# Performance work log

Hardware: AMD Instinct MI355X
Metric: run time of the kernel (lower is better)

## Reference

```python
import jax, jax.numpy as jnp
import numpy as np

D = 256      # word_embd_size
V = 32000    # vocab_size_w
B, T, J = 32, 512, 128


def _gru_dir(x, wih, whh, bih, bhh):
    # x: (B, T, D); torch GRU cell convention
    def step(h, xt):
        gi = xt @ wih.T + bih            # (B, 3D)
        gh = h @ whh.T + bhh
        i_r, i_z, i_n = jnp.split(gi, 3, axis=-1)
        h_r, h_z, h_n = jnp.split(gh, 3, axis=-1)
        r = jax.nn.sigmoid(i_r + h_r)
        z = jax.nn.sigmoid(i_z + h_z)
        n = jnp.tanh(i_n + r * h_n)
        h_new = (1.0 - z) * n + z * h
        return h_new, h_new
    h0 = jnp.zeros((x.shape[0], D), dtype=x.dtype)
    _, ys = jax.lax.scan(step, h0, jnp.swapaxes(x, 0, 1))
    return jnp.swapaxes(ys, 0, 1)         # (B, T, D)


def _bigru(x, wih_f, whh_f, bih_f, bhh_f, wih_b, whh_b, bih_b, bhh_b):
    fwd = _gru_dir(x, wih_f, whh_f, bih_f, bhh_f)
    bwd = jnp.flip(_gru_dir(jnp.flip(x, 1), wih_b, whh_b, bih_b, bhh_b), 1)
    return jnp.concatenate([fwd, bwd], axis=-1)   # (B, T, 2D)


def _cmnt_sim(ctx, cmnt_e, action, w2):
    # Fused form of: S = W2_ha(cat(ctx_ex * cmnt_ex, action_ex)) over (B,T,J,2D+1)
    # S[b,t,j] = sum_d ctx[b,t,d]*cmnt[b,j,d]*w2[d] + action[b,t]*w2[2D]
    S = jnp.einsum('btd,bjd->btj', ctx * w2[:2 * D], cmnt_e)
    S = S + action.astype(ctx.dtype)[:, :, None] * w2[2 * D]
    b = jax.nn.softmax(jnp.max(S, axis=2), axis=-1)   # (B, T)
    return jnp.einsum('bt,btj->bj', b, S)             # (B, J)


def setup_inputs() -> dict:
    key = jax.random.key(0)
    ks = jax.random.split(key, 20)
    s = 1.0 / np.sqrt(D)
    u = lambda k, shape: jax.random.uniform(k, shape, minval=-s, maxval=s, dtype=jnp.float32)
    return {
        'cmnt': jax.random.randint(ks[0], (B, J), 0, V),
        'src_token': jax.random.randint(ks[1], (B, T), 0, V),
        'tgt_token': jax.random.randint(ks[2], (B, T), 0, V),
        'src_action': jax.random.randint(ks[3], (B, T), 0, 2),
        'tgt_action': jax.random.randint(ks[4], (B, T), 0, 2),
        'emb': jax.random.normal(ks[5], (V, D), dtype=jnp.float32) * 0.02,
        'wih_f': u(ks[6], (3 * D, D)), 'whh_f': u(ks[7], (3 * D, D)),
        'bih_f': u(ks[8], (3 * D,)),  'bhh_f': u(ks[9], (3 * D,)),
        'wih_b': u(ks[10], (3 * D, D)), 'whh_b': u(ks[11], (3 * D, D)),
        'bih_b': u(ks[12], (3 * D,)),  'bhh_b': u(ks[13], (3 * D,)),
        'w2': u(ks[14], (2 * D + 1,)),
        'rank_w': u(ks[15], (2 * J, 1)),
        'rank_b': u(ks[16], (1,)),
    }


def reference(cmnt, src_token, tgt_token, src_action, tgt_action, emb,
              wih_f, whh_f, bih_f, bhh_f, wih_b, whh_b, bih_b, bhh_b,
              w2, rank_w, rank_b):
    gru = lambda x: _bigru(x, wih_f, whh_f, bih_f, bhh_f, wih_b, whh_b, bih_b, bhh_b)
    e_src = gru(emb[src_token])    # (B, T, 2D)
    e_tgt = gru(emb[tgt_token])    # (B, T, 2D)
    e_cmnt = gru(emb[cmnt])        # (B, J, 2D)
    S_src = _cmnt_sim(e_src, e_cmnt, src_action, w2)
    S_tgt = _cmnt_sim(e_tgt, e_cmnt, tgt_action, w2)
    S_diff = jnp.concatenate([S_src, S_tgt], axis=1)   # (B, 2J)
    result = S_diff @ rank_w + rank_b                   # (B, 1)
    return result, S_diff
```

## Files before the change

kernel.cpp:

```cpp
#include <hip/hip_runtime.h>
#include <math.h>

#define DD   256
#define TTT  512
#define JJJ  128
#define BBB  32
#define NC   1536
#define ROWS_ALL 36864

typedef _Float16 v2h __attribute__((ext_vector_type(2)));
typedef _Float16 v4h __attribute__((ext_vector_type(4)));
typedef short short8 __attribute__((ext_vector_type(8)));
typedef float f32x4 __attribute__((ext_vector_type(4)));

#if __has_builtin(__builtin_amdgcn_fdot2)
#define FDOT2(a, b, c) __builtin_amdgcn_fdot2((a), (b), (c), false)
#else
#define FDOT2(a, b, c) ((float)(a)[0] * (float)(b)[0] + ((float)(a)[1] * (float)(b)[1] + (c)))
#endif

__device__ __forceinline__ short f2bf(float f) {
    unsigned u = __float_as_uint(f);
    unsigned r = (u + 0x7FFFu + ((u >> 16) & 1u)) >> 16;
    return (short)r;
}

__global__ __launch_bounds__(256) void prep_kernel(
    const int* __restrict__ cmnt, const int* __restrict__ src_tok, const int* __restrict__ tgt_tok,
    const float* __restrict__ wih_f, const float* __restrict__ wih_b,
    const float* __restrict__ whh_f, const float* __restrict__ whh_b,
    const float* __restrict__ bih_f, const float* __restrict__ bih_b,
    const float* __restrict__ bhh_f, const float* __restrict__ bhh_b,
    int* __restrict__ tok_all, float* __restrict__ whhT,
    float* __restrict__ bihc, float* __restrict__ bhhc, short* __restrict__ Bt)
{
    const int idx = blockIdx.x * blockDim.x + threadIdx.x;
    const int stride = gridDim.x * blockDim.x;
    for (int i = idx; i < ROWS_ALL; i += stride)
        tok_all[i] = (i < 16384) ? src_tok[i] : (i < 32768) ? tgt_tok[i - 16384] : cmnt[i - 32768];
    for (int i = idx; i < 256 * NC; i += stride) {
        const int k = i / NC, c = i % NC;
        whhT[i] = (c < 768) ? whh_f[(size_t)c * 256 + k] : whh_b[(size_t)(c - 768) * 256 + k];
    }
    for (int i = idx; i < 393216; i += stride)
        Bt[i] = f2bf(i < 196608 ? wih_f[i] : wih_b[i - 196608]);
    for (int i = idx; i < NC; i += stride) {
        bihc[i] = (i < 768) ? bih_f[i] : bih_b[i - 768];
        bhhc[i] = (i < 768) ? bhh_f[i] : bhh_b[i - 768];
    }
}

__global__ __launch_bounds__(256) void gatherA_kernel(
    const int* __restrict__ tok, int row_start, int nrows,
    const float* __restrict__ emb, short* __restrict__ A)
{
    const int idx = blockIdx.x * blockDim.x + threadIdx.x;
    const int stride = gridDim.x * blockDim.x;
    const int ngroups = nrows * 64;
    for (int g = idx; g < ngroups; g += stride) {
        const int i = g >> 6;
        const int kq = (g & 63) << 2;
        const float4 v = *(const float4*)(emb + (size_t)tok[row_start + i] * 256 + kq);
        short4 s;
        s.x = f2bf(v.x); s.y = f2bf(v.y); s.z = f2bf(v.z); s.w = f2bf(v.w);
        *(short4*)(A + (size_t)i * 256 + kq) = s;
    }
}

#define LP 40
__global__ __launch_bounds__(256) void gi_mfma(
    const short* __restrict__ A, const short* __restrict__ Bt,
    const float* __restrict__ bihc, _Float16* __restrict__ gi)
{
    __shared__ __align__(16) short As[128 * LP];
    __shared__ __align__(16) short Bs[128 * LP];
    const int tid = threadIdx.x;
    const int wave = tid >> 6, lane = tid & 63;
    const int quad = lane >> 4, l16 = lane & 15;
    const int m0 = blockIdx.x * 128, n0 = blockIdx.y * 128;
    const int wm = (wave & 1) * 64, wn = (wave >> 1) * 64;

    const int sr = tid >> 2;
    const int sk = (tid & 3) * 8;
    const short* ga0 = A  + (size_t)(m0 + sr) * 256 + sk;
    const short* ga1 = A  + (size_t)(m0 + sr + 64) * 256 + sk;
    const short* gb0 = Bt + (size_t)(n0 + sr) * 256 + sk;
    const short* gb1 = Bt + (size_t)(n0 + sr + 64) * 256 + sk;

    f32x4 acc[4][4];
    #pragma unroll
    for (int i = 0; i < 4; ++i)
        #pragma unroll
        for (int j = 0; j < 4; ++j) acc[i][j] = (f32x4){0.f, 0.f, 0.f, 0.f};

    for (int k0 = 0; k0 < 256; k0 += 32) {
        const short8 a0 = *(const short8*)(ga0 + k0);
        const short8 a1 = *(const short8*)(ga1 + k0);
        const short8 b0 = *(const short8*)(gb0 + k0);
        const short8 b1 = *(const short8*)(gb1 + k0);
        __syncthreads();
        *(short8*)&As[sr * LP + sk] = a0;
        *(short8*)&As[(sr + 64) * LP + sk] = a1;
        *(short8*)&Bs[sr * LP + sk] = b0;
        *(short8*)&Bs[(sr + 64) * LP + sk] = b1;
        __syncthreads();
        short8 af[4], bf[4];
        #pragma unroll
        for (int i = 0; i < 4; ++i)
            af[i] = *(const short8*)&As[(wm + i * 16 + l16) * LP + quad * 8];
        #pragma unroll
        for (int j = 0; j < 4; ++j)
            bf[j] = *(const short8*)&Bs[(wn + j * 16 + l16) * LP + quad * 8];
        #pragma unroll
        for (int i = 0; i < 4; ++i)
            #pragma unroll
            for (int j = 0; j < 4; ++j)
                acc[i][j] = __builtin_amdgcn_mfma_f32_16x16x32_bf16(af[i], bf[j], acc[i][j], 0, 0, 0);
    }

    #pragma unroll
    for (int j = 0; j < 4; ++j) {
        const int col = n0 + wn + j * 16 + l16;
        const float bias = bihc[col];
        #pragma unroll
        for (int i = 0; i < 4; ++i) {
            const int r0 = m0 + wm + i * 16 + quad * 4;
            #pragma unroll
            for (int reg = 0; reg < 4; ++reg)
                gi[(size_t)(r0 + reg) * NC + col] = (_Float16)(acc[i][j][reg] + bias);
        }
    }
}

__global__ __launch_bounds__(512, 2) void gru_kernel(
    const _Float16* __restrict__ gi0, const _Float16* __restrict__ gi1, const _Float16* __restrict__ gi2,
    const float* __restrict__ whhT, const float* __restrict__ bhhc,
    _Float16* __restrict__ e_src, _Float16* __restrict__ e_tgt, _Float16* __restrict__ e_cmnt,
    int chain_base)
{
    const int chain = chain_base + (int)(blockIdx.x >> 5);
    const int b = (int)(blockIdx.x & 31);
    const int seq = chain >> 1, dir = chain & 1;
    const int Tlen = (seq == 2) ? JJJ : TTT;
    const _Float16* gi = (seq == 0) ? gi0 : (seq == 1) ? gi1 : gi2;
    _Float16* e = (seq == 0) ? e_src : (seq == 1) ? e_tgt : e_cmnt;

    const int tid = threadIdx.x;
    const int j = tid & 255;
    const int q = tid >> 8;
    const int cb = dir * 768;

    __shared__ __align__(16) v2h h2s[128];
    __shared__ float parts[3][256];

    v2h wr2[64], wz2[64], wn2[64];
    {
        const float* wb = whhT + (size_t)(q * 128) * NC + cb + j;
        #pragma unroll
        for (int p = 0; p < 64; ++p) {
            v2h a, bzv, c;
            a[0]   = (_Float16)wb[0];        a[1]   = (_Float16)wb[NC];
            bzv[0] = (_Float16)wb[256];      bzv[1] = (_Float16)wb[NC + 256];
            c[0]   = (_Float16)wb[512];      c[1]   = (_Float16)wb[NC + 512];
            wr2[p] = a; wz2[p] = bzv; wn2[p] = c;
            wb += 2 * NC;
        }
    }
    const float br  = bhhc[cb + j];
    const float bzb = bhhc[cb + 256 + j];
    const float bnb = bhhc[cb + 512 + j];

    float hprev = 0.f;
    if (q == 0 && (j & 1) == 0) {
        v2h z0; z0[0] = (_Float16)0.f; z0[1] = (_Float16)0.f;
        h2s[j >> 1] = z0;
    }
    __syncthreads();

    const int t0i = dir ? (Tlen - 1) : 0;
    const long tstep = dir ? -1 : 1;
    const _Float16* girow = gi + (size_t)(b * Tlen + t0i) * NC + cb;
    _Float16* eptr = e + (size_t)(b * Tlen + t0i) * 512 + (dir << 8) + j;
    const long gstep = tstep * NC;
    const long estep = tstep * 512;

    for (int s = 0; s < Tlen; ++s) {
        float gr_ = 0.f, gz_ = 0.f, gn_ = 0.f;
        if (q == 0) {
            gr_ = (float)girow[j];
            gz_ = (float)girow[256 + j];
            gn_ = (float)girow[512 + j];
        }

        float ar = 0.f, az = 0.f, an = 0.f;
        const v2h* hbase = &h2s[q * 64];
        #pragma unroll
        for (int c = 0; c < 16; ++c) {
            union { float4 f; v2h h[4]; } U;
            U.f = *(const float4*)&hbase[c * 4];
            #pragma unroll
            for (int p = 0; p < 4; ++p) {
                ar = FDOT2(wr2[c * 4 + p], U.h[p], ar);
                az = FDOT2(wz2[c * 4 + p], U.h[p], az);
                an = FDOT2(wn2[c * 4 + p], U.h[p], an);
            }
        }
        if (q == 1) { parts[0][j] = ar; parts[1][j] = az; parts[2][j] = an; }
        __syncthreads();

        if (q == 0) {
            const float sr = ar + parts[0][j] + br;
            const float sz = az + parts[1][j] + bzb;
            const float sn = an + parts[2][j] + bnb;
            const float r = 1.f / (1.f + __expf(-(gr_ + sr)));
            const float z = 1.f / (1.f + __expf(-(gz_ + sz)));
            const float n = tanhf(gn_ + r * sn);
            const float hnew = (1.f - z) * n + z * hprev;
            hprev = hnew;
            *eptr = (_Float16)hnew;
            const float hnb = __shfl_xor(hnew, 1);
            if ((j & 1) == 0) {
                v2h hv; hv[0] = (_Float16)hnew; hv[1] = (_Float16)hnb;
                h2s[j >> 1] = hv;
            }
        }
        girow += gstep;
        eptr += estep;
        __syncthreads();
    }
}

__global__ __launch_bounds__(256) void sim_gemm(
    const _Float16* __restrict__ e_src, const _Float16* __restrict__ e_tgt,
    const _Float16* __restrict__ e_cmnt, const float* __restrict__ w2,
    const int* __restrict__ src_action, const int* __restrict__ tgt_action,
    float* __restrict__ S, float* __restrict__ rowmaxP)
{
    const int seq = (int)(blockIdx.z >> 5);
    const int b = (int)(blockIdx.z & 31);
    const int t0 = blockIdx.x * 64;
    const int j0 = blockIdx.y * 64;
    const _Float16* ctx = ((seq == 0) ? e_src : e_tgt) + (size_t)b * 512 * 512;
    const _Float16* ec = e_cmnt + (size_t)b * 128 * 512;
    const int* act = (seq == 0) ? src_action : tgt_action;

    __shared__ __align__(16) float As[16][68];
    __shared__ __align__(16) float Bs[16][68];
    const int tid = threadIdx.x;
    const int lr = tid >> 2;
    const int lk = (tid & 3) << 2;
    const int ty = tid >> 4, tx = tid & 15;
    float acc[4][4];
    #pragma unroll
    for (int i = 0; i < 4; ++i)
        #pragma unroll
        for (int q = 0; q < 4; ++q) acc[i][q] = 0.f;

    for (int k0 = 0; k0 < 512; k0 += 16) {
        const float4 w4 = *(const float4*)(w2 + k0 + lk);
        const v4h a4 = *(const v4h*)(ctx + (size_t)(t0 + lr) * 512 + k0 + lk);
        const v4h b4 = *(const v4h*)(ec + (size_t)(j0 + lr) * 512 + k0 + lk);
        __syncthreads();
        As[lk + 0][lr] = (float)a4[0] * w4.x; As[lk + 1][lr] = (float)a4[1] * w4.y;
        As[lk + 2][lr] = (float)a4[2] * w4.z; As[lk + 3][lr] = (float)a4[3] * w4.w;
        Bs[lk + 0][lr] = (float)b4[0]; Bs[lk + 1][lr] = (float)b4[1];
        Bs[lk + 2][lr] = (float)b4[2]; Bs[lk + 3][lr] = (float)b4[3];
        __syncthreads();
        #pragma unroll
        for (int kk = 0; kk < 16; ++kk) {
            const float4 av = *(const float4*)&As[kk][ty * 4];
            const float4 bv = *(const float4*)&Bs[kk][tx * 4];
            float a[4] = {av.x, av.y, av.z, av.w};
            float bb[4] = {bv.x, bv.y, bv.z, bv.w};
            #pragma unroll
            for (int i = 0; i < 4; ++i)
                #pragma unroll
                for (int q = 0; q < 4; ++q) acc[i][q] = fmaf(a[i], bb[q], acc[i][q]);
        }
    }
    const float w2a = w2[512];
    #pragma unroll
    for (int i = 0; i < 4; ++i) {
        const int t = t0 + ty * 4 + i;
        const float aterm = (float)act[b * 512 + t] * w2a;
        float4 o;
        o.x = acc[i][0] + aterm; o.y = acc[i][1] + aterm;
        o.z = acc[i][2] + aterm; o.w = acc[i][3] + aterm;
        *(float4*)(S + ((size_t)((seq * 32 + b) * 512 + t)) * 128 + j0 + tx * 4) = o;
        float m = fmaxf(fmaxf(o.x, o.y), fmaxf(o.z, o.w));
        m = fmaxf(m, __shfl_xor(m, 1));
        m = fmaxf(m, __shfl_xor(m, 2));
        m = fmaxf(m, __shfl_xor(m, 4));
        m = fmaxf(m, __shfl_xor(m, 8));
        if (tx == 0)
            rowmaxP[(size_t)blockIdx.y * 32768 + (seq * 32 + b) * 512 + t] = m;
    }
}

__global__ __launch_bounds__(256) void softmax_kernel(const float* __restrict__ rowmaxP, float* __restrict__ bw)
{
    const int base = blockIdx.x * 512;
    const int tid = threadIdx.x;
    __shared__ float red[256];
    const float v0 = fmaxf(rowmaxP[base + tid], rowmaxP[32768 + base + tid]);
    const float v1 = fmaxf(rowmaxP[base + 256 + tid], rowmaxP[32768 + base + 256 + tid]);
    red[tid] = fmaxf(v0, v1);
    __syncthreads();
    for (int off = 128; off > 0; off >>= 1) {
        if (tid < off) red[tid] = fmaxf(red[tid], red[tid + off]);
        __syncthreads();
    }
    const float M = red[0];
    __syncthreads();
    const float e0 = __expf(v0 - M), e1 = __expf(v1 - M);
    red[tid] = e0 + e1;
    __syncthreads();
    for (int off = 128; off > 0; off >>= 1) {
        if (tid < off) red[tid] += red[tid + off];
        __syncthreads();
    }
    const float inv = 1.f / red[0];
    bw[base + tid] = e0 * inv;
    bw[base + 256 + tid] = e1 * inv;
}

__global__ __launch_bounds__(256) void weighted_kernel(
    const float* __restrict__ S, const float* __restrict__ bw, float* __restrict__ outSP)
{
    const int sb = blockIdx.x;
    const int ch = blockIdx.y;
    const int tid = threadIdx.x;
    const int j = tid & 127, half = tid >> 7;
    const float* Sb = S + (size_t)sb * 512 * 128;
    const float* w = bw + sb * 512;
    const int tb = ch * 64 + half * 32;
    float acc = 0.f;
    for (int t = tb; t < tb + 32; ++t)
        acc = fmaf(w[t], Sb[(size_t)t * 128 + j], acc);
    __shared__ float red[256];
    red[tid] = acc;
    __syncthreads();
    if (half == 0) outSP[(size_t)ch * 8192 + sb * 128 + j] = red[j] + red[128 + j];
}

__global__ __launch_bounds__(256) void final_kernel(
    const float* __restrict__ outSP, const float* __restrict__ rank_w,
    const float* __restrict__ rank_b, float* __restrict__ out)
{
    __shared__ float sArr[8192];
    const int tid = threadIdx.x;
    for (int q = tid; q < 8192; q += 256) {
        float s = 0.f;
        #pragma unroll
        for (int c = 0; c < 8; ++c) s += outSP[(size_t)c * 8192 + q];
        sArr[q] = s;
    }
    __syncthreads();
    for (int q = tid; q < 8192; q += 256) {
        const int b = q >> 8, c = q & 255;
        out[32 + q] = (c < 128) ? sArr[b * 128 + c] : sArr[4096 + b * 128 + (c - 128)];
    }
    if (tid < 32) {
        float acc = rank_b[0];
        for (int c = 0; c < 128; ++c) acc = fmaf(sArr[tid * 128 + c], rank_w[c], acc);
        for (int c = 0; c < 128; ++c) acc = fmaf(sArr[4096 + tid * 128 + c], rank_w[128 + c], acc);
        out[tid] = acc;
    }
}

extern "C" void kernel_launch(void* const* d_in, const int* in_sizes, int n_in,
                              void* d_out, int out_size, void* d_ws, size_t ws_size,
                              hipStream_t stream)
{
    const int* cmnt       = (const int*)d_in[0];
    const int* src_token  = (const int*)d_in[1];
    const int* tgt_token  = (const int*)d_in[2];
    const int* src_action = (const int*)d_in[3];
    const int* tgt_action = (const int*)d_in[4];
    const float* emb    = (const float*)d_in[5];
    const float* wih_f  = (const float*)d_in[6];
    const float* whh_f  = (const float*)d_in[7];
    const float* bih_f  = (const float*)d_in[8];
    const float* bhh_f  = (const float*)d_in[9];
    const float* wih_b  = (const float*)d_in[10];
    const float* whh_b  = (const float*)d_in[11];
    const float* bih_b  = (const float*)d_in[12];
    const float* bhh_b  = (const float*)d_in[13];
    const float* w2     = (const float*)d_in[14];
    const float* rank_w = (const float*)d_in[15];
    const float* rank_b = (const float*)d_in[16];
    float* out = (float*)d_out;

    float* ws = (float*)d_ws;
    size_t off = 0;
    int*   tok_all = (int*)(ws + off); off += 36864;
    short* Bt_bf16 = (short*)(ws + off); off += 196608;
    float* whhT   = ws + off; off += 393216;
    float* bihc   = ws + off; off += 1536;
    float* bhhc   = ws + off; off += 1536;
    float* rowmaxP = ws + off; off += 65536;
    float* bw     = ws + off; off += 32768;
    float* outSP  = ws + off; off += 65536;
    _Float16* e_src  = (_Float16*)(ws + off); off += 4194304;
    _Float16* e_tgt  = (_Float16*)(ws + off); off += 4194304;
    _Float16* e_cmnt = (_Float16*)(ws + off); off += 1048576;
    float* S      = ws + off; off += 4194304;
    _Float16* gih = (_Float16*)(ws + off);
    const size_t avail = ws_size / 4 - off;
    const bool planP = avail >= 28311552ULL;

    hipLaunchKernelGGL(prep_kernel, dim3(512), dim3(256), 0, stream,
        cmnt, src_token, tgt_token, wih_f, wih_b, whh_f, whh_b,
        bih_f, bih_b, bhh_f, bhh_b, tok_all, whhT, bihc, bhhc, Bt_bf16);

    if (planP) {
        short* A = (short*)e_src;
        hipLaunchKernelGGL(gatherA_kernel, dim3(4096), dim3(256), 0, stream,
            tok_all, 0, 36864, emb, A);
        hipLaunchKernelGGL(gi_mfma, dim3(288, 12), dim3(256), 0, stream,
            A, Bt_bf16, bihc, gih);
        hipLaunchKernelGGL(gru_kernel, dim3(192), dim3(512), 0, stream,
            gih, gih + (size_t)16384 * NC, gih + (size_t)32768 * NC,
            whhT, bhhc, e_src, e_tgt, e_cmnt, 0);
    } else {
        short* A = (short*)S;
        const int starts[3] = {0, 16384, 32768};
        const int nrows[3]  = {16384, 16384, 4096};
        for (int sq = 0; sq < 3; ++sq) {
            hipLaunchKernelGGL(gatherA_kernel, dim3(4096), dim3(256), 0, stream,
                tok_all, starts[sq], nrows[sq], emb, A);
            hipLaunchKernelGGL(gi_mfma, dim3(nrows[sq] / 128, 12), dim3(256), 0, stream,
                A, Bt_bf16, bihc, gih);
            hipLaunchKernelGGL(gru_kernel, dim3(64), dim3(512), 0, stream,
                gih, gih, gih, whhT, bhhc, e_src, e_tgt, e_cmnt, 2 * sq);
        }
    }

    hipLaunchKernelGGL(sim_gemm, dim3(8, 2, 64), dim3(256), 0, stream,
        e_src, e_tgt, e_cmnt, w2, src_action, tgt_action, S, rowmaxP);
    hipLaunchKernelGGL(softmax_kernel, dim3(64), dim3(256), 0, stream, rowmaxP, bw);
    hipLaunchKernelGGL(weighted_kernel, dim3(64, 8), dim3(256), 0, stream, S, bw, outSP);
    hipLaunchKernelGGL(final_kernel, dim3(1), dim3(256), 0, stream, outSP, rank_w, rank_b, out);
}
```

Measured before the change: 895.8 us.

## Port similarity GEMM to fp16 MFMA, defer GRU stores, use expf tanh

Replaces the scalar-FMA similarity GEMM with a 128x128-tile MFMA kernel using fp16 operands, with w2 pre-converted to fp16 and multiplied into the context rows in half precision. In the GRU recurrence, each step's global store of h is deferred to the start of the next step so it overlaps the next gate loads. tanhf is replaced by an exp-based formula. These cut FMA throughput cost and per-step latency on the sequential GRU path, but the fp16 product of context and w2 and the fast tanh lower accuracy.

```diff
diff --git a/kernel.cpp b/kernel.cpp
--- a/kernel.cpp
+++ b/kernel.cpp
@@ -10,6 +10,7 @@
 
 typedef _Float16 v2h __attribute__((ext_vector_type(2)));
 typedef _Float16 v4h __attribute__((ext_vector_type(4)));
+typedef _Float16 v8h __attribute__((ext_vector_type(8)));
 typedef short short8 __attribute__((ext_vector_type(8)));
 typedef float f32x4 __attribute__((ext_vector_type(4)));
 
@@ -31,8 +32,10 @@
     const float* __restrict__ whh_f, const float* __restrict__ whh_b,
     const float* __restrict__ bih_f, const float* __restrict__ bih_b,
     const float* __restrict__ bhh_f, const float* __restrict__ bhh_b,
+    const float* __restrict__ w2,
     int* __restrict__ tok_all, float* __restrict__ whhT,
-    float* __restrict__ bihc, float* __restrict__ bhhc, short* __restrict__ Bt)
+    float* __restrict__ bihc, float* __restrict__ bhhc, short* __restrict__ Bt,
+    _Float16* __restrict__ w2h)
 {
     const int idx = blockIdx.x * blockDim.x + threadIdx.x;
     const int stride = gridDim.x * blockDim.x;
@@ -48,6 +51,8 @@
         bihc[i] = (i < 768) ? bih_f[i] : bih_b[i - 768];
         bhhc[i] = (i < 768) ? bhh_f[i] : bhh_b[i - 768];
     }
+    for (int i = idx; i < 512; i += stride)
+        w2h[i] = (_Float16)w2[i];
 }
 
 __global__ __launch_bounds__(256) void gatherA_kernel(
@@ -184,9 +189,13 @@
     const long gstep = tstep * NC;
     const long estep = tstep * 512;
 
+    _Float16* pptr = eptr;
+    float pval = 0.f;
+
     for (int s = 0; s < Tlen; ++s) {
         float gr_ = 0.f, gz_ = 0.f, gn_ = 0.f;
         if (q == 0) {
+            if (s > 0) *pptr = (_Float16)pval;
             gr_ = (float)girow[j];
             gz_ = (float)girow[256 + j];
             gn_ = (float)girow[512 + j];
@@ -214,10 +223,12 @@
             const float sn = an + parts[2][j] + bnb;
             const float r = 1.f / (1.f + __expf(-(gr_ + sr)));
             const float z = 1.f / (1.f + __expf(-(gz_ + sz)));
-            const float n = tanhf(gn_ + r * sn);
+            const float xa = gn_ + r * sn;
+            const float texp = __expf(2.f * xa);
+            const float n = 1.f - 2.f / (texp + 1.f);
             const float hnew = (1.f - z) * n + z * hprev;
             hprev = hnew;
-            *eptr = (_Float16)hnew;
+            pptr = eptr; pval = hnew;
             const float hnb = __shfl_xor(hnew, 1);
             if ((j & 1) == 0) {
                 v2h hv; hv[0] = (_Float16)hnew; hv[1] = (_Float16)hnb;
@@ -228,72 +239,92 @@
         eptr += estep;
         __syncthreads();
     }
-}
-
-__global__ __launch_bounds__(256) void sim_gemm(
+    if (q == 0) *pptr = (_Float16)pval;
+}
+
+__global__ __launch_bounds__(256) void sim_mfma(
     const _Float16* __restrict__ e_src, const _Float16* __restrict__ e_tgt,
-    const _Float16* __restrict__ e_cmnt, const float* __restrict__ w2,
+    const _Float16* __restrict__ e_cmnt, const _Float16* __restrict__ w2h,
+    const float* __restrict__ w2,
     const int* __restrict__ src_action, const int* __restrict__ tgt_action,
     float* __restrict__ S, float* __restrict__ rowmaxP)
 {
-    const int seq = (int)(blockIdx.z >> 5);
-    const int b = (int)(blockIdx.z & 31);
-    const int t0 = blockIdx.x * 64;
-    const int j0 = blockIdx.y * 64;
+    const int sb = (int)blockIdx.z;
+    const int seq = sb >> 5, b = sb & 31;
+    const int t0 = blockIdx.x * 128;
     const _Float16* ctx = ((seq == 0) ? e_src : e_tgt) + (size_t)b * 512 * 512;
     const _Float16* ec = e_cmnt + (size_t)b * 128 * 512;
     const int* act = (seq == 0) ? src_action : tgt_action;
 
-    __shared__ __align__(16) float As[16][68];
-    __shared__ __align__(16) float Bs[16][68];
-    const int tid = threadIdx.x;
-    const int lr = tid >> 2;
-    const int lk = (tid & 3) << 2;
-    const int ty = tid >> 4, tx = tid & 15;
-    float acc[4][4];
+    __shared__ __align__(16) _Float16 As[128 * LP];
+    __shared__ __align__(16) _Float16 Bs[128 * LP];
+    const int tid = threadIdx.x;
+    const int wave = tid >> 6, lane = tid & 63;
+    const int quad = lane >> 4, l16 = lane & 15;
+    const int wm = (wave & 1) * 64, wn = (wave >> 1) * 64;
+    const int sr = tid >> 2;
+    const int sk = (tid & 3) * 8;
+
+    const _Float16* ga0 = ctx + (size_t)(t0 + sr) * 512 + sk;
+    const _Float16* ga1 = ctx + (size_t)(t0 + sr + 64) * 512 + sk;
+    const _Float16* gb0 = ec + (size_t)sr * 512 + sk;
+    const _Float16* gb1 = ec + (size_t)(sr + 64) * 512 + sk;
+
+    f32x4 acc[4][4];
     #pragma unroll
     for (int i = 0; i < 4; ++i)
         #pragma unroll
-        for (int q = 0; q < 4; ++q) acc[i][q] = 0.f;
-
-    for (int k0 = 0; k0 < 512; k0 += 16) {
-        const float4 w4 = *(const float4*)(w2 + k0 + lk);
-        const v4h a4 = *(const v4h*)(ctx + (size_t)(t0 + lr) * 512 + k0 + lk);
-        const v4h b4 = *(const v4h*)(ec + (size_t)(j0 + lr) * 512 + k0 + lk);
-        __syncthreads();
-        As[lk + 0][lr] = (float)a4[0] * w4.x; As[lk + 1][lr] = (float)a4[1] * w4.y;
-        As[lk + 2][lr] = (float)a4[2] * w4.z; As[lk + 3][lr] = (float)a4[3] * w4.w;
-        Bs[lk + 0][lr] = (float)b4[0]; Bs[lk + 1][lr] = (float)b4[1];
-        Bs[lk + 2][lr] = (float)b4[2]; Bs[lk + 3][lr] = (float)b4[3];
-        __syncthreads();
-        #pragma unroll
-        for (int kk = 0; kk < 16; ++kk) {
-            const float4 av = *(const float4*)&As[kk][ty * 4];
-            const float4 bv = *(const float4*)&Bs[kk][tx * 4];
-            float a[4] = {av.x, av.y, av.z, av.w};
-            float bb[4] = {bv.x, bv.y, bv.z, bv.w};
+        for (int j = 0; j < 4; ++j) acc[i][j] = (f32x4){0.f, 0.f, 0.f, 0.f};
+
+    for (int k0 = 0; k0 < 512; k0 += 32) {
+        v8h a0 = *(const v8h*)(ga0 + k0);
+        v8h a1 = *(const v8h*)(ga1 + k0);
+        const v8h b0 = *(const v8h*)(gb0 + k0);
+        const v8h b1 = *(const v8h*)(gb1 + k0);
+        const v8h w8 = *(const v8h*)(w2h + k0 + sk);
+        a0 = a0 * w8;
+        a1 = a1 * w8;
+        __syncthreads();
+        *(v8h*)&As[sr * LP + sk] = a0;
+        *(v8h*)&As[(sr + 64) * LP + sk] = a1;
+        *(v8h*)&Bs[sr * LP + sk] = b0;
+        *(v8h*)&Bs[(sr + 64) * LP + sk] = b1;
+        __syncthreads();
+        v8h af[4], bf[4];
+        #pragma unroll
+        for (int i = 0; i < 4; ++i)
+            af[i] = *(const v8h*)&As[(wm + i * 16 + l16) * LP + quad * 8];
+        #pragma unroll
+        for (int j = 0; j < 4; ++j)
+            bf[j] = *(const v8h*)&Bs[(wn + j * 16 + l16) * LP + quad * 8];
+        #pragma unroll
+        for (int i = 0; i < 4; ++i)
             #pragma unroll
-            for (int i = 0; i < 4; ++i)
-                #pragma unroll
-                for (int q = 0; q < 4; ++q) acc[i][q] = fmaf(a[i], bb[q], acc[i][q]);
-        }
-    }
+            for (int j = 0; j < 4; ++j)
+                acc[i][j] = __builtin_amdgcn_mfma_f32_16x16x32_f16(af[i], bf[j], acc[i][j], 0, 0, 0);
+    }
+
     const float w2a = w2[512];
     #pragma unroll
     for (int i = 0; i < 4; ++i) {
-        const int t = t0 + ty * 4 + i;
-        const float aterm = (float)act[b * 512 + t] * w2a;
-        float4 o;
-        o.x = acc[i][0] + aterm; o.y = acc[i][1] + aterm;
-        o.z = acc[i][2] + aterm; o.w = acc[i][3] + aterm;
-        *(float4*)(S + ((size_t)((seq * 32 + b) * 512 + t)) * 128 + j0 + tx * 4) = o;
-        float m = fmaxf(fmaxf(o.x, o.y), fmaxf(o.z, o.w));
-        m = fmaxf(m, __shfl_xor(m, 1));
-        m = fmaxf(m, __shfl_xor(m, 2));
-        m = fmaxf(m, __shfl_xor(m, 4));
-        m = fmaxf(m, __shfl_xor(m, 8));
-        if (tx == 0)
-            rowmaxP[(size_t)blockIdx.y * 32768 + (seq * 32 + b) * 512 + t] = m;
+        #pragma unroll
+        for (int reg = 0; reg < 4; ++reg) {
+            const int t = t0 + wm + i * 16 + quad * 4 + reg;
+            const float aterm = (float)act[b * 512 + t] * w2a;
+            float m = -1e30f;
+            #pragma unroll
+            for (int j = 0; j < 4; ++j) {
+                const float v = acc[i][j][reg] + aterm;
+                S[((size_t)(sb * 512 + t)) * 128 + wn + j * 16 + l16] = v;
+                m = fmaxf(m, v);
+            }
+            m = fmaxf(m, __shfl_xor(m, 1));
+            m = fmaxf(m, __shfl_xor(m, 2));
+            m = fmaxf(m, __shfl_xor(m, 4));
+            m = fmaxf(m, __shfl_xor(m, 8));
+            if (l16 == 0)
+                rowmaxP[(size_t)(wave >> 1) * 32768 + sb * 512 + t] = m;
+        }
     }
 }
 
@@ -398,6 +429,7 @@
     float* whhT   = ws + off; off += 393216;
     float* bihc   = ws + off; off += 1536;
     float* bhhc   = ws + off; off += 1536;
+    _Float16* w2h = (_Float16*)(ws + off); off += 256;
     float* rowmaxP = ws + off; off += 65536;
     float* bw     = ws + off; off += 32768;
     float* outSP  = ws + off; off += 65536;
@@ -411,7 +443,7 @@
 
     hipLaunchKernelGGL(prep_kernel, dim3(512), dim3(256), 0, stream,
         cmnt, src_token, tgt_token, wih_f, wih_b, whh_f, whh_b,
-        bih_f, bih_b, bhh_f, bhh_b, tok_all, whhT, bihc, bhhc, Bt_bf16);
+        bih_f, bih_b, bhh_f, bhh_b, w2, tok_all, whhT, bihc, bhhc, Bt_bf16, w2h);
 
     if (planP) {
         short* A = (short*)e_src;
@@ -436,8 +468,8 @@
         }
     }
 
-    hipLaunchKernelGGL(sim_gemm, dim3(8, 2, 64), dim3(256), 0, stream,
-        e_src, e_tgt, e_cmnt, w2, src_action, tgt_action, S, rowmaxP);
+    hipLaunchKernelGGL(sim_mfma, dim3(4, 1, 64), dim3(256), 0, stream,
+        e_src, e_tgt, e_cmnt, w2h, w2, src_action, tgt_action, S, rowmaxP);
     hipLaunchKernelGGL(softmax_kernel, dim3(64), dim3(256), 0, stream, rowmaxP, bw);
     hipLaunchKernelGGL(weighted_kernel, dim3(64, 8), dim3(256), 0, stream, S, bw, outSP);
     hipLaunchKernelGGL(final_kernel, dim3(1), dim3(256), 0, stream, outSP, rank_w, rank_b, out);
```

Result: faster. 844.8 us (median of 2 runs) (-5.7%).
